# Performance work log

Hardware: AMD Instinct MI355X
Metric: run time of the kernel (lower is better)

The kernel has to match this reference:

```python
import jax, jax.numpy as jnp
import numpy as np

K = 512
U = 2
TEMP_BERN = 0.67
TEMP_CAT = 0.67
EULER = 0.5772156649015329
EPS = 1e-8
UEPS = 1e-6


def setup_inputs() -> dict:
    key = jax.random.key(0)
    ks = jax.random.split(key, 3)
    B, D = 16384, 1024
    inputs = jax.random.normal(ks[0], (B, D), jnp.float32)
    # glorot-normal-ish init for mW
    mW = jax.random.normal(ks[1], (D, K * U), jnp.float32) * jnp.sqrt(2.0 / (D + K * U))
    sW = jnp.full((D, K * U), -5.0, jnp.float32)
    conc1 = jnp.full((K,), 2.0, jnp.float32)
    conc0 = jnp.full((K,), 0.5453, jnp.float32)
    t_pi = jax.random.uniform(ks[2], (D, K), jnp.float32, 4.0, 5.0)
    biases = jnp.full((K * U,), 0.1, jnp.float32)
    return {"inputs": inputs, "mW": mW, "sW": sW, "conc1": conc1,
            "conc0": conc0, "t_pi": t_pi, "biases": biases}


def _uniform(k, shape):
    return jax.random.uniform(k, shape, jnp.float32, UEPS, 1.0 - UEPS)


def reference(inputs, mW, sW, conc1, conc0, t_pi, biases):
    rk = jax.random.split(jax.random.key(42), 4)

    # --- reparameterized weights W = mW + eps * softplus(sW) ---
    sW_sp = jax.nn.softplus(sW)
    eps = jax.lax.stop_gradient(jax.random.normal(rk[0], mW.shape, jnp.float32))
    W = mW + eps * sW_sp
    kl_weights = -0.5 * jnp.mean(2.0 * sW_sp - jnp.square(mW) - jnp.square(sW_sp) + 1.0)
    layer_loss = kl_weights / 60000.0

    # --- IBP: relaxed Bernoulli sample of t_pi ([D, K]) ---
    u = _uniform(rk[1], t_pi.shape)
    logistic = jnp.log(u) - jnp.log1p(-u)
    z_sample = jax.nn.sigmoid((t_pi + logistic) / TEMP_BERN)  # bin_concrete_sample
    z = jnp.tile(z_sample, (1, U))  # [D, K*U], column order u*K+k (as in TF code)

    # Kumaraswamy stick-breaking prior: cumprod along axis 0 (TF default)
    a_sp = jax.nn.softplus(conc1)  # [K]
    b_sp = jax.nn.softplus(conc0)  # [K]
    uk = _uniform(rk[2], t_pi.shape)
    q_u = jnp.power(1.0 - jnp.power(uk, 1.0 / b_sp), 1.0 / a_sp)  # kumaraswamy_sample
    prior_pi = jnp.cumprod(q_u, axis=0)
    q = jax.nn.sigmoid(t_pi)
    kl_z = jnp.sum(q * (jnp.log(q + EPS) - jnp.log(prior_pi + EPS)))

    # KL(Kumaraswamy(a,b) || Beta(1,1)); (beta-1) series term vanishes
    kl_sticks = jnp.sum(((a_sp - 1.0) / a_sp) * (-EULER - jax.scipy.special.digamma(b_sp) - 1.0 / b_sp)
                        + jnp.log(a_sp * b_sp + EPS) - (b_sp - 1.0) / b_sp)
    layer_loss = layer_loss + kl_sticks + kl_z

    W = z * W
    out = inputs @ W + biases  # [B, K*U]

    # --- LWTA activation via Gumbel-softmax over U competitors ---
    logits = out.reshape(-1, K, U)  # [B, K, U]
    g = -jnp.log(-jnp.log(_uniform(rk[3], logits.shape)))
    xi = jax.nn.softmax((logits + g) / TEMP_CAT, axis=-1)  # concrete_sample
    out_act = (logits * xi).reshape(out.shape)
    q_xi = jax.nn.softmax(logits, axis=-1)
    kl_xi = jnp.mean(jnp.sum(q_xi * (jnp.log(q_xi + EPS) - jnp.log(1.0 / U)), axis=1))
    layer_loss = layer_loss + kl_xi

    return out_act, layer_loss
```

## Files before the change

### kernel.cpp

```cpp
#include <hip/hip_runtime.h>
#include <stdint.h>
#include <math.h>

#define B_N   16384
#define D_N   1024
#define K_N   512
#define KU_N  1024
#define EPS_F 1e-8f
#define TEMP  0.67f
#define EULERC 0.5772156649015329f

#define HEPS  524288
#define HU    262144
#define HG    8388608

typedef uint32_t u32;
typedef __attribute__((ext_vector_type(4))) float f32x4;
typedef __attribute__((ext_vector_type(4))) unsigned int u32x4;
typedef __attribute__((ext_vector_type(8))) __bf16 bf16x8;

#define TF_ROT(x, r) (((x) << (r)) | ((x) >> (32 - (r))))

__host__ __device__ static inline void threefry2x32(u32 k0, u32 k1,
                                                    u32 x0, u32 x1,
                                                    u32* o0, u32* o1) {
  u32 ks2 = k0 ^ k1 ^ 0x1BD11BDAu;
  x0 += k0; x1 += k1;
  x0 += x1; x1 = TF_ROT(x1, 13); x1 ^= x0;
  x0 += x1; x1 = TF_ROT(x1, 15); x1 ^= x0;
  x0 += x1; x1 = TF_ROT(x1, 26); x1 ^= x0;
  x0 += x1; x1 = TF_ROT(x1, 6);  x1 ^= x0;
  x0 += k1; x1 += ks2 + 1u;
  x0 += x1; x1 = TF_ROT(x1, 17); x1 ^= x0;
  x0 += x1; x1 = TF_ROT(x1, 29); x1 ^= x0;
  x0 += x1; x1 = TF_ROT(x1, 16); x1 ^= x0;
  x0 += x1; x1 = TF_ROT(x1, 24); x1 ^= x0;
  x0 += ks2; x1 += k0 + 2u;
  x0 += x1; x1 = TF_ROT(x1, 13); x1 ^= x0;
  x0 += x1; x1 = TF_ROT(x1, 15); x1 ^= x0;
  x0 += x1; x1 = TF_ROT(x1, 26); x1 ^= x0;
  x0 += x1; x1 = TF_ROT(x1, 6);  x1 ^= x0;
  x0 += k0; x1 += k1 + 3u;
  x0 += x1; x1 = TF_ROT(x1, 17); x1 ^= x0;
  x0 += x1; x1 = TF_ROT(x1, 29); x1 ^= x0;
  x0 += x1; x1 = TF_ROT(x1, 16); x1 ^= x0;
  x0 += x1; x1 = TF_ROT(x1, 24); x1 ^= x0;
  x0 += k1; x1 += ks2 + 4u;
  x0 += x1; x1 = TF_ROT(x1, 13); x1 ^= x0;
  x0 += x1; x1 = TF_ROT(x1, 15); x1 ^= x0;
  x0 += x1; x1 = TF_ROT(x1, 26); x1 ^= x0;
  x0 += x1; x1 = TF_ROT(x1, 6);  x1 ^= x0;
  x0 += ks2; x1 += k0 + 5u;
  *o0 = x0; *o1 = x1;
}

__device__ static inline float bits_to_u01(u32 b) {
  u32 f = (b >> 9) | 0x3f800000u;
  return __uint_as_float(f) - 1.0f;
}
__device__ static inline float unif_f(u32 b, float lo, float hi) {
  float f = bits_to_u01(b);
  return fmaxf(lo, f * (hi - lo) + lo);
}
__device__ static inline float erfinv_f(float x) {
  float w = -log1pf(-x * x);
  float p;
  if (w < 5.f) {
    w -= 2.5f;
    p = 2.81022636e-08f;
    p = fmaf(p, w, 3.43273939e-07f);
    p = fmaf(p, w, -3.5233877e-06f);
    p = fmaf(p, w, -4.39150654e-06f);
    p = fmaf(p, w, 0.00021858087f);
    p = fmaf(p, w, -0.00125372503f);
    p = fmaf(p, w, -0.00417768164f);
    p = fmaf(p, w, 0.246640727f);
    p = fmaf(p, w, 1.50140941f);
  } else {
    w = sqrtf(w) - 3.f;
    p = -0.000200214257f;
    p = fmaf(p, w, 0.000100950558f);
    p = fmaf(p, w, 0.00134934322f);
    p = fmaf(p, w, -0.00367342844f);
    p = fmaf(p, w, 0.00573950773f);
    p = fmaf(p, w, -0.0076224613f);
    p = fmaf(p, w, 0.00943887047f);
    p = fmaf(p, w, 1.00167406f);
    p = fmaf(p, w, 2.83297682f);
  }
  return p * x;
}
__device__ static inline float softplus_f(float x) {
  return fmaxf(x, 0.f) + log1pf(expf(-fabsf(x)));
}
__device__ static inline float rcp_f(float x) { return __builtin_amdgcn_rcpf(x); }
__device__ static inline float sigmoid_fast(float x) {
  return rcp_f(1.f + __expf(-x));
}
__device__ static inline float digamma_f(float x) {
  float r = 0.f;
  while (x < 6.f) { r -= 1.f / x; x += 1.f; }
  float inv = 1.f / x, inv2 = inv * inv;
  return r + logf(x) - 0.5f * inv
       - inv2 * (1.f / 12.f - inv2 * (1.f / 120.f - inv2 * (1.f / 252.f)));
}
__device__ static inline unsigned short f2bf_rne(float x) {
  u32 u = __float_as_uint(x);
  u32 r = (u + 0x7fffu + ((u >> 16) & 1u)) >> 16;
  return (unsigned short)r;
}
__device__ static inline u32 cvt_pk_bf16(float lo, float hi) {
  u32 r;
  asm("v_cvt_pk_bf16_f32 %0, %1, %2" : "=v"(r) : "v"(lo), "v"(hi));
  return r;
}
__device__ static inline void gload_lds16(const void* g, void* l) {
  __builtin_amdgcn_global_load_lds(
      (const __attribute__((address_space(1))) u32*)g,
      (__attribute__((address_space(3))) u32*)l, 16, 0, 0);
}

__device__ static inline float block_sum(float v) {
  __shared__ float sm[16];
  int lane = threadIdx.x & 63;
  int wid = threadIdx.x >> 6;
  #pragma unroll
  for (int o = 32; o > 0; o >>= 1) v += __shfl_down(v, o, 64);
  if (lane == 0) sm[wid] = v;
  __syncthreads();
  float s = 0.f;
  if (threadIdx.x == 0) {
    int nw = (blockDim.x + 63) >> 6;
    s = sm[0];
    for (int w = 1; w < nw; ++w) s += sm[w];
  }
  return s;
}

__global__ void k_init(const float* __restrict__ conc1,
                       const float* __restrict__ conc0,
                       float* __restrict__ invA, float* __restrict__ invB,
                       float* gacc) {
  int k = threadIdx.x;
  float a = softplus_f(conc1[k]);
  float b = softplus_f(conc0[k]);
  invA[k] = 1.f / a;
  invB[k] = 1.f / b;
  float s = ((a - 1.f) / a) * (-EULERC - digamma_f(b) - 1.f / b)
          + logf(a * b + EPS_F) - (b - 1.f) / b;
  float t = block_sum(s);
  if (threadIdx.x == 0) { gacc[0] = 0.f; gacc[1] = t; gacc[2] = 0.f; }
}

__global__ __launch_bounds__(256) void k_klz_a(const float* __restrict__ invA,
                                               const float* __restrict__ invB,
                                               float* __restrict__ P,
                                               u32 qk0, u32 qk1) {
  int idx = blockIdx.x * 256 + threadIdx.x;
  int c = idx >> 9, k = idx & (K_N - 1);
  float iA = invA[k], iB = invB[k];
  float p = 1.f;
  int d0 = c << 4;
  for (int d = d0; d < d0 + 16; ++d) {
    int n = (d << 9) + k;
    u32 x0 = (n < HU) ? (u32)n : (u32)(n - HU);
    u32 o0, o1;
    threefry2x32(qk0, qk1, x0, x0 + HU, &o0, &o1);
    u32 bits = (n < HU) ? o0 : o1;
    float u = unif_f(bits, 1e-6f, 1.f - 1e-6f);
    p *= powf(1.f - powf(u, iB), iA);
  }
  P[idx] = p;
}

__global__ __launch_bounds__(256) void k_klz_b(const float* __restrict__ t_pi,
                                               const float* __restrict__ invA,
                                               const float* __restrict__ invB,
                                               const float* __restrict__ P,
                                               float* gacc,
                                               u32 qk0, u32 qk1) {
  int idx = blockIdx.x * 256 + threadIdx.x;
  int c = idx >> 9, k = idx & (K_N - 1);
  float iA = invA[k], iB = invB[k];
  float prior = 1.f;
  for (int c2 = 0; c2 < c; ++c2) prior *= P[(c2 << 9) + k];
  float s = 0.f;
  int d0 = c << 4;
  for (int d = d0; d < d0 + 16; ++d) {
    int n = (d << 9) + k;
    u32 x0 = (n < HU) ? (u32)n : (u32)(n - HU);
    u32 o0, o1;
    threefry2x32(qk0, qk1, x0, x0 + HU, &o0, &o1);
    u32 bits = (n < HU) ? o0 : o1;
    float u = unif_f(bits, 1e-6f, 1.f - 1e-6f);
    prior *= powf(1.f - powf(u, iB), iA);
    float q = sigmoid_fast(t_pi[n]);
    s += q * (__logf(q + EPS_F) - __logf(prior + EPS_F));
  }
  float t = block_sum(s);
  if (threadIdx.x == 0) atomicAdd(&gacc[1], t);
}

__global__ __launch_bounds__(256) void k_wbuildT(const float* __restrict__ mW,
                                                 const float* __restrict__ sW,
                                                 const float* __restrict__ t_pi,
                                                 unsigned short* __restrict__ WzT,
                                                 float* __restrict__ gacc,
                                                 u32 ek0, u32 ek1,
                                                 u32 uk0, u32 uk1) {
  __shared__ unsigned short tile[64][65];
  int dt = (int)blockIdx.x >> 4;
  int jt = (int)blockIdx.x & 15;
  int d0 = dt << 6, j0 = jt << 6;
  int tj = threadIdx.x & 63;
  int tr = threadIdx.x >> 6;
  int j = j0 + tj;
  int kk = j & (K_N - 1);
  bool lowD = (dt < 8);
  float klw = 0.f;
  #pragma unroll 4
  for (int rr = 0; rr < 16; ++rr) {
    int dl = (rr << 2) + tr;
    int d = d0 + dl;
    int n = (d << 10) + j;
    u32 x0 = lowD ? (u32)n : (u32)(n - HEPS);
    u32 o0, o1;
    threefry2x32(ek0, ek1, x0, x0 + HEPS, &o0, &o1);
    u32 ebits = lowD ? o0 : o1;
    int nz = (d << 9) + kk;
    u32 zx0 = lowD ? (u32)nz : (u32)(nz - HU);
    u32 z0, z1;
    threefry2x32(uk0, uk1, zx0, zx0 + HU, &z0, &z1);
    u32 zbits = lowD ? z0 : z1;
    float u = unif_f(zbits, 1e-6f, 1.f - 1e-6f);
    float logistic = __logf(u) - log1pf(-u);
    float z = sigmoid_fast((t_pi[nz] + logistic) * (1.f / TEMP));
    float un = unif_f(ebits, -0.99999994f, 1.0f);
    float epsn = 1.41421356f * erfinv_f(un);
    float m = mW[n], sp = softplus_f(sW[n]);
    tile[tj][dl] = f2bf_rne(z * (m + epsn * sp));
    klw += 2.f * sp - m * m - sp * sp + 1.f;
  }
  __syncthreads();
  #pragma unroll 4
  for (int rr = 0; rr < 16; ++rr) {
    int jl = (rr << 2) + tr;
    WzT[(size_t)(j0 + jl) * D_N + d0 + tj] = tile[jl][tj];
  }
  float t = block_sum(klw);
  if (threadIdx.x == 0) atomicAdd(&gacc[0], t);
}

#define GBM 128
#define GBN 128
#define GBK 64

__global__ __launch_bounds__(256) void k_gemm(const float* __restrict__ A,
                                              const unsigned short* __restrict__ Bt,
                                              const float* __restrict__ bias,
                                              float* __restrict__ C) {
  __shared__ __align__(16) unsigned short As[2][GBM * GBK];
  __shared__ __align__(16) unsigned short Bs[2][GBN * GBK];

  int f = (int)blockIdx.x;
  int wk = (f & 7) * 128 + (f >> 3);
  const int brow = (wk >> 3) * GBM;
  const int bcol = (wk & 7) * GBN;

  const int tid = threadIdx.x;
  const int lane = tid & 63;
  const int w = tid >> 6;

  const int ar = tid >> 1;
  const float* gA = A + (size_t)(brow + ar) * D_N + ((tid & 1) << 5);
  const int cb = (tid & 1) << 2;
  int aoff[4];
  #pragma unroll
  for (int i = 0; i < 4; ++i)
    aoff[i] = (ar << 7) + (((cb + i) ^ (ar & 7)) << 4);

  const int bcl = tid >> 3;
  const unsigned short* gB = Bt + (size_t)(bcol + bcl) * D_N
                           + (((tid & 7) ^ (bcl & 7)) << 3);
  const int bdst = (w << 10);

  f32x4 acc[4][4];
  #pragma unroll
  for (int m = 0; m < 4; ++m)
    #pragma unroll
    for (int n = 0; n < 4; ++n) acc[m][n] = (f32x4){0.f, 0.f, 0.f, 0.f};

  const int wr = (w >> 1) << 6;
  const int wc = (w & 1) << 6;
  const int fr = lane & 15;
  const int kg = lane >> 4;

  f32x4 av[8];

  #pragma unroll
  for (int j = 0; j < 8; ++j) av[j] = *(const f32x4*)(gA + (j << 2));
  #pragma unroll
  for (int q = 0; q < 4; ++q)
    gload_lds16(gB + (size_t)(q * 32) * D_N, (char*)Bs[0] + q * 4096 + bdst);
  __builtin_amdgcn_sched_barrier(0);
  #pragma unroll
  for (int i = 0; i < 4; ++i) {
    u32x4 p;
    p.x = cvt_pk_bf16(av[2 * i].x, av[2 * i].y);
    p.y = cvt_pk_bf16(av[2 * i].z, av[2 * i].w);
    p.z = cvt_pk_bf16(av[2 * i + 1].x, av[2 * i + 1].y);
    p.w = cvt_pk_bf16(av[2 * i + 1].z, av[2 * i + 1].w);
    *(u32x4*)((char*)As[0] + aoff[i]) = p;
  }
  #pragma unroll
  for (int j = 0; j < 8; ++j) av[j] = *(const f32x4*)(gA + GBK + (j << 2));

  for (int t = 0; t < 15; ++t) {
    const int cur = t & 1;
    char* curA = (char*)As + (cur << 14);
    char* curB = (char*)Bs + (cur << 14);
    char* altA = (char*)As + ((cur ^ 1) << 14);
    char* altB = (char*)Bs + ((cur ^ 1) << 14);

    asm volatile("s_waitcnt vmcnt(8) lgkmcnt(0)" ::: "memory");
    __builtin_amdgcn_s_barrier();

    {
      const unsigned short* gBn = gB + ((t + 1) << 6);
      #pragma unroll
      for (int q = 0; q < 4; ++q)
        gload_lds16(gBn + (size_t)(q * 32) * D_N, altB + q * 4096 + bdst);
    }
    __builtin_amdgcn_sched_barrier(0);

    #pragma unroll
    for (int h = 0; h < 2; ++h) {
      bf16x8 af[4];
      #pragma unroll
      for (int m = 0; m < 4; ++m) {
        int row = wr + m * 16 + fr;
        af[m] = *(const bf16x8*)(curA + (row << 7) + ((((h << 2) + kg) ^ (row & 7)) << 4));
      }
      #pragma unroll
      for (int n = 0; n < 4; ++n) {
        int col = wc + n * 16 + fr;
        bf16x8 bf = *(const bf16x8*)(curB + (col << 7) + ((((h << 2) + kg) ^ (col & 7)) << 4));
        #pragma unroll
        for (int m = 0; m < 4; ++m)
          acc[m][n] = __builtin_amdgcn_mfma_f32_16x16x32_bf16(af[m], bf, acc[m][n], 0, 0, 0);
      }
    }

    #pragma unroll
    for (int i = 0; i < 4; ++i) {
      u32x4 p;
      p.x = cvt_pk_bf16(av[2 * i].x, av[2 * i].y);
      p.y = cvt_pk_bf16(av[2 * i].z, av[2 * i].w);
      p.z = cvt_pk_bf16(av[2 * i + 1].x, av[2 * i + 1].y);
      p.w = cvt_pk_bf16(av[2 * i + 1].z, av[2 * i + 1].w);
      *(u32x4*)(altA + aoff[i]) = p;
    }
    if (t < 14) {
      const float* g = gA + ((t + 2) << 6);
      #pragma unroll
      for (int j = 0; j < 8; ++j) av[j] = *(const f32x4*)(g + (j << 2));
    }
  }

  asm volatile("s_waitcnt vmcnt(0) lgkmcnt(0)" ::: "memory");
  __builtin_amdgcn_s_barrier();
  {
    char* curA = (char*)As + (1 << 14);
    char* curB = (char*)Bs + (1 << 14);
    #pragma unroll
    for (int h = 0; h < 2; ++h) {
      bf16x8 af[4];
      #pragma unroll
      for (int m = 0; m < 4; ++m) {
        int row = wr + m * 16 + fr;
        af[m] = *(const bf16x8*)(curA + (row << 7) + ((((h << 2) + kg) ^ (row & 7)) << 4));
      }
      #pragma unroll
      for (int n = 0; n < 4; ++n) {
        int col = wc + n * 16 + fr;
        bf16x8 bf = *(const bf16x8*)(curB + (col << 7) + ((((h << 2) + kg) ^ (col & 7)) << 4));
        #pragma unroll
        for (int m = 0; m < 4; ++m)
          acc[m][n] = __builtin_amdgcn_mfma_f32_16x16x32_bf16(af[m], bf, acc[m][n], 0, 0, 0);
      }
    }
  }

  #pragma unroll
  for (int n = 0; n < 4; ++n) {
    int col = bcol + wc + n * 16 + fr;
    float bv = bias[col];
    #pragma unroll
    for (int m = 0; m < 4; ++m) {
      int rowb = brow + wr + m * 16 + (kg << 2);
      C[(size_t)(rowb + 0) * KU_N + col] = acc[m][n].x + bv;
      C[(size_t)(rowb + 1) * KU_N + col] = acc[m][n].y + bv;
      C[(size_t)(rowb + 2) * KU_N + col] = acc[m][n].z + bv;
      C[(size_t)(rowb + 3) * KU_N + col] = acc[m][n].w + bv;
    }
  }
}

__device__ static inline float lwta_pair(float v0, float v1, u32 ba, u32 bb,
                                         float* o0, float* o1) {
  float u0 = unif_f(ba, 1e-6f, 1.f - 1e-6f);
  float u1 = unif_f(bb, 1e-6f, 1.f - 1e-6f);
  float g0 = -__logf(-__logf(u0));
  float g1 = -__logf(-__logf(u1));
  const float it = 1.f / TEMP;
  float d = ((v1 + g1) - (v0 + g0)) * it;
  float xi0 = rcp_f(1.f + __expf(d));
  float xi1 = 1.f - xi0;
  *o0 = v0 * xi0;
  *o1 = v1 * xi1;
  float qd = v1 - v0;
  float q0 = rcp_f(1.f + __expf(qd));
  float q1 = 1.f - q0;
  const float LOG2F = 0.6931471805599453f;
  return q0 * (__logf(q0 + EPS_F) + LOG2F) + q1 * (__logf(q1 + EPS_F) + LOG2F);
}

__global__ __launch_bounds__(256) void k_epi(float* __restrict__ C,
                                             float* __restrict__ partial,
                                             u32 gk0, u32 gk1) {
  int idx = blockIdx.x * 256 + threadIdx.x;
  int b = idx >> 9;
  int c2 = (idx & 511) << 1;
  size_t p0 = (size_t)b * KU_N + c2;
  size_t p1 = p0 + (size_t)8192 * KU_N;
  float2 r0 = *(const float2*)&C[p0];
  float2 r1 = *(const float2*)&C[p1];
  u32 m = ((u32)b << 10) | (u32)c2;
  u32 x0a, x1a, x0b, x1b;
  threefry2x32(gk0, gk1, m,      m + HG,      &x0a, &x1a);
  threefry2x32(gk0, gk1, m + 1u, m + 1u + HG, &x0b, &x1b);
  float2 w0, w1;
  float kl = lwta_pair(r0.x, r0.y, x0a, x0b, &w0.x, &w0.y)
           + lwta_pair(r1.x, r1.y, x1a, x1b, &w1.x, &w1.y);
  *(float2*)&C[p0] = w0;
  *(float2*)&C[p1] = w1;
  float t = block_sum(kl);
  if (threadIdx.x == 0) partial[blockIdx.x] = t;
}

#define NPART 16384
__global__ __launch_bounds__(256) void k_final(const float* __restrict__ gacc,
                                               const float* __restrict__ partial,
                                               float* __restrict__ out_loss) {
  float s = 0.f;
  for (int i = threadIdx.x; i < NPART; i += 256) s += partial[i];
  float t = block_sum(s);
  if (threadIdx.x == 0) {
    float kl_weights = -0.5f * (gacc[0] * (1.f / 1048576.f));
    out_loss[0] = kl_weights / 60000.f + gacc[1] + t * (1.f / 32768.f);
  }
}

extern "C" void kernel_launch(void* const* d_in, const int* in_sizes, int n_in,
                              void* d_out, int out_size, void* d_ws, size_t ws_size,
                              hipStream_t stream) {
  (void)in_sizes; (void)n_in; (void)out_size; (void)ws_size;
  const float* inputs = (const float*)d_in[0];
  const float* mW     = (const float*)d_in[1];
  const float* sW     = (const float*)d_in[2];
  const float* conc1  = (const float*)d_in[3];
  const float* conc0  = (const float*)d_in[4];
  const float* t_pi   = (const float*)d_in[5];
  const float* biases = (const float*)d_in[6];
  float* out = (float*)d_out;

  u32 a[4], b[4];
  for (int i = 0; i < 4; ++i)
    threefry2x32(0u, 42u, (u32)i, (u32)(i + 4), &a[i], &b[i]);
  u32 e_k0 = a[0], e_k1 = a[1];
  u32 u_k0 = a[2], u_k1 = a[3];
  u32 q_k0 = b[0], q_k1 = b[1];
  u32 g_k0 = b[2], g_k1 = b[3];

  char* wsb = (char*)d_ws;
  unsigned short* WzT = (unsigned short*)wsb;
  float* P       = (float*)(wsb + (2u << 20));
  float* invA    = (float*)(wsb + (2u << 20) + (128u << 10));
  float* invB    = (float*)(wsb + (2u << 20) + (130u << 10));
  float* gacc    = (float*)(wsb + (2u << 20) + (132u << 10));
  float* partial = (float*)(wsb + (2u << 20) + (136u << 10));

  hipLaunchKernelGGL(k_init, dim3(1), dim3(512), 0, stream,
                     conc1, conc0, invA, invB, gacc);
  hipLaunchKernelGGL(k_klz_a, dim3(128), dim3(256), 0, stream,
                     invA, invB, P, q_k0, q_k1);
  hipLaunchKernelGGL(k_klz_b, dim3(128), dim3(256), 0, stream,
                     t_pi, invA, invB, P, gacc, q_k0, q_k1);
  hipLaunchKernelGGL(k_wbuildT, dim3(256), dim3(256), 0, stream,
                     mW, sW, t_pi, WzT, gacc, e_k0, e_k1, u_k0, u_k1);
  hipLaunchKernelGGL(k_gemm, dim3(1024), dim3(256), 0, stream,
                     inputs, WzT, biases, out);
  hipLaunchKernelGGL(k_epi, dim3(NPART), dim3(256), 0, stream,
                     out, partial, g_k0, g_k1);
  hipLaunchKernelGGL(k_final, dim3(1), dim3(256), 0, stream,
                     gacc, partial, out + 16777216);
}
```

Before: 218.0 us.

## Enlarge GEMM block tile to 256x256 with 512 threads and restructured barriers

The GEMM moves from 128x128 tiles with 256 threads to 256x256 tiles with 512 threads. Each wave now computes a 128x64 sub-tile with 8x4 MFMA accumulators, and the grid shrinks to 256 blocks. The wait and barrier move to the end of each loop iteration, and s_setprio raises wave priority around the MFMA section. The larger tile cuts global and LDS traffic per FLOP, at the cost of more registers and LDS per block and only 256 blocks to spread across the CUs.

```diff
diff --git a/kernel.cpp b/kernel.cpp
--- a/kernel.cpp
+++ b/kernel.cpp
@@ -251,21 +251,21 @@
   if (threadIdx.x == 0) atomicAdd(&gacc[0], t);
 }
 
-#define GBM 128
-#define GBN 128
-#define GBK 64
-
-__global__ __launch_bounds__(256) void k_gemm(const float* __restrict__ A,
-                                              const unsigned short* __restrict__ Bt,
-                                              const float* __restrict__ bias,
-                                              float* __restrict__ C) {
-  __shared__ __align__(16) unsigned short As[2][GBM * GBK];
-  __shared__ __align__(16) unsigned short Bs[2][GBN * GBK];
+#define TBM 256
+#define TBN 256
+#define TBK 64
+
+__global__ __launch_bounds__(512, 2) void k_gemm(const float* __restrict__ A,
+                                                 const unsigned short* __restrict__ Bt,
+                                                 const float* __restrict__ bias,
+                                                 float* __restrict__ C) {
+  __shared__ __align__(16) unsigned short As[2][TBM * TBK];
+  __shared__ __align__(16) unsigned short Bs[2][TBN * TBK];
 
   int f = (int)blockIdx.x;
-  int wk = (f & 7) * 128 + (f >> 3);
-  const int brow = (wk >> 3) * GBM;
-  const int bcol = (wk & 7) * GBN;
+  int wk = (f & 7) * 32 + (f >> 3);
+  const int brow = (wk >> 2) * TBM;
+  const int bcol = (wk & 3) * TBN;
 
   const int tid = threadIdx.x;
   const int lane = tid & 63;
@@ -284,14 +284,14 @@
                            + (((tid & 7) ^ (bcl & 7)) << 3);
   const int bdst = (w << 10);
 
-  f32x4 acc[4][4];
-  #pragma unroll
-  for (int m = 0; m < 4; ++m)
+  f32x4 acc[8][4];
+  #pragma unroll
+  for (int m = 0; m < 8; ++m)
     #pragma unroll
     for (int n = 0; n < 4; ++n) acc[m][n] = (f32x4){0.f, 0.f, 0.f, 0.f};
 
-  const int wr = (w >> 1) << 6;
-  const int wc = (w & 1) << 6;
+  const int wrow = (w >> 2) << 7;
+  const int wcol = (w & 3) << 6;
   const int fr = lane & 15;
   const int kg = lane >> 4;
 
@@ -301,7 +301,7 @@
   for (int j = 0; j < 8; ++j) av[j] = *(const f32x4*)(gA + (j << 2));
   #pragma unroll
   for (int q = 0; q < 4; ++q)
-    gload_lds16(gB + (size_t)(q * 32) * D_N, (char*)Bs[0] + q * 4096 + bdst);
+    gload_lds16(gB + (size_t)(q * 64) * D_N, (char*)Bs[0] + q * 8192 + bdst);
   __builtin_amdgcn_sched_barrier(0);
   #pragma unroll
   for (int i = 0; i < 4; ++i) {
@@ -313,43 +313,44 @@
     *(u32x4*)((char*)As[0] + aoff[i]) = p;
   }
   #pragma unroll
-  for (int j = 0; j < 8; ++j) av[j] = *(const f32x4*)(gA + GBK + (j << 2));
+  for (int j = 0; j < 8; ++j) av[j] = *(const f32x4*)(gA + TBK + (j << 2));
+  asm volatile("s_waitcnt vmcnt(8) lgkmcnt(0)" ::: "memory");
+  __builtin_amdgcn_s_barrier();
 
   for (int t = 0; t < 15; ++t) {
     const int cur = t & 1;
-    char* curA = (char*)As + (cur << 14);
-    char* curB = (char*)Bs + (cur << 14);
-    char* altA = (char*)As + ((cur ^ 1) << 14);
-    char* altB = (char*)Bs + ((cur ^ 1) << 14);
-
-    asm volatile("s_waitcnt vmcnt(8) lgkmcnt(0)" ::: "memory");
-    __builtin_amdgcn_s_barrier();
+    char* curA = (char*)As + (cur << 15);
+    char* curB = (char*)Bs + (cur << 15);
+    char* altA = (char*)As + ((cur ^ 1) << 15);
+    char* altB = (char*)Bs + ((cur ^ 1) << 15);
 
     {
       const unsigned short* gBn = gB + ((t + 1) << 6);
       #pragma unroll
       for (int q = 0; q < 4; ++q)
-        gload_lds16(gBn + (size_t)(q * 32) * D_N, altB + q * 4096 + bdst);
+        gload_lds16(gBn + (size_t)(q * 64) * D_N, altB + q * 8192 + bdst);
     }
     __builtin_amdgcn_sched_barrier(0);
 
+    __builtin_amdgcn_s_setprio(1);
     #pragma unroll
     for (int h = 0; h < 2; ++h) {
-      bf16x8 af[4];
+      bf16x8 af[8];
       #pragma unroll
-      for (int m = 0; m < 4; ++m) {
-        int row = wr + m * 16 + fr;
+      for (int m = 0; m < 8; ++m) {
+        int row = wrow + m * 16 + fr;
         af[m] = *(const bf16x8*)(curA + (row << 7) + ((((h << 2) + kg) ^ (row & 7)) << 4));
       }
       #pragma unroll
       for (int n = 0; n < 4; ++n) {
-        int col = wc + n * 16 + fr;
+        int col = wcol + n * 16 + fr;
         bf16x8 bf = *(const bf16x8*)(curB + (col << 7) + ((((h << 2) + kg) ^ (col & 7)) << 4));
         #pragma unroll
-        for (int m = 0; m < 4; ++m)
+        for (int m = 0; m < 8; ++m)
           acc[m][n] = __builtin_amdgcn_mfma_f32_16x16x32_bf16(af[m], bf, acc[m][n], 0, 0, 0);
       }
     }
+    __builtin_amdgcn_s_setprio(0);
 
     #pragma unroll
     for (int i = 0; i < 4; ++i) {
@@ -365,27 +366,30 @@
       #pragma unroll
       for (int j = 0; j < 8; ++j) av[j] = *(const f32x4*)(g + (j << 2));
     }
-  }
-
-  asm volatile("s_waitcnt vmcnt(0) lgkmcnt(0)" ::: "memory");
+
+    asm volatile("s_waitcnt vmcnt(8) lgkmcnt(0)" ::: "memory");
+    __builtin_amdgcn_s_barrier();
+  }
+
+  asm volatile("s_waitcnt vmcnt(0)" ::: "memory");
   __builtin_amdgcn_s_barrier();
   {
-    char* curA = (char*)As + (1 << 14);
-    char* curB = (char*)Bs + (1 << 14);
+    char* curA = (char*)As + (1 << 15);
+    char* curB = (char*)Bs + (1 << 15);
     #pragma unroll
     for (int h = 0; h < 2; ++h) {
-      bf16x8 af[4];
+      bf16x8 af[8];
       #pragma unroll
-      for (int m = 0; m < 4; ++m) {
-        int row = wr + m * 16 + fr;
+      for (int m = 0; m < 8; ++m) {
+        int row = wrow + m * 16 + fr;
         af[m] = *(const bf16x8*)(curA + (row << 7) + ((((h << 2) + kg) ^ (row & 7)) << 4));
       }
       #pragma unroll
       for (int n = 0; n < 4; ++n) {
-        int col = wc + n * 16 + fr;
+        int col = wcol + n * 16 + fr;
         bf16x8 bf = *(const bf16x8*)(curB + (col << 7) + ((((h << 2) + kg) ^ (col & 7)) << 4));
         #pragma unroll
-        for (int m = 0; m < 4; ++m)
+        for (int m = 0; m < 8; ++m)
           acc[m][n] = __builtin_amdgcn_mfma_f32_16x16x32_bf16(af[m], bf, acc[m][n], 0, 0, 0);
       }
     }
@@ -393,11 +397,11 @@
 
   #pragma unroll
   for (int n = 0; n < 4; ++n) {
-    int col = bcol + wc + n * 16 + fr;
+    int col = bcol + wcol + n * 16 + fr;
     float bv = bias[col];
     #pragma unroll
-    for (int m = 0; m < 4; ++m) {
-      int rowb = brow + wr + m * 16 + (kg << 2);
+    for (int m = 0; m < 8; ++m) {
+      int rowb = brow + wrow + m * 16 + (kg << 2);
       C[(size_t)(rowb + 0) * KU_N + col] = acc[m][n].x + bv;
       C[(size_t)(rowb + 1) * KU_N + col] = acc[m][n].y + bv;
       C[(size_t)(rowb + 2) * KU_N + col] = acc[m][n].z + bv;
@@ -498,7 +502,7 @@
                      t_pi, invA, invB, P, gacc, q_k0, q_k1);
   hipLaunchKernelGGL(k_wbuildT, dim3(256), dim3(256), 0, stream,
                      mW, sW, t_pi, WzT, gacc, e_k0, e_k1, u_k0, u_k1);
-  hipLaunchKernelGGL(k_gemm, dim3(1024), dim3(256), 0, stream,
+  hipLaunchKernelGGL(k_gemm, dim3(256), dim3(512), 0, stream,
                      inputs, WzT, biases, out);
   hipLaunchKernelGGL(k_epi, dim3(NPART), dim3(256), 0, stream,
                      out, partial, g_k0, g_k1);
```

Result: faster. 189.4 us (-13.1%).
